# Kernel optimization log

Measured on AMD Instinct MI355X. Metric: run time of the kernel, lower is better.

The kernel has to match this reference:

```python
import jax, jax.numpy as jnp
import numpy as np

N_EMBD = 1024
HEAD_SIZE = 64
B, T = 8, 2048


def setup_inputs() -> dict:
    key = jax.random.key(0)
    kx, kq, kk, kv = jax.random.split(key, 4)
    s = 1.0 / np.sqrt(N_EMBD)  # ~ torch Linear init scale
    return {
        "x": jax.random.normal(kx, (B, T, N_EMBD), dtype=jnp.float32),
        "Wq": jax.random.normal(kq, (N_EMBD, HEAD_SIZE), dtype=jnp.float32) * s,
        "Wk": jax.random.normal(kk, (N_EMBD, HEAD_SIZE), dtype=jnp.float32) * s,
        "Wv": jax.random.normal(kv, (N_EMBD, HEAD_SIZE), dtype=jnp.float32) * s,
    }


def reference(x, Wq, Wk, Wv):
    # x: [B,T,C]; single-head causal self-attention (dropout p=0.0 / eval)
    q = jnp.einsum("btc,cd->btd", x, Wq)
    k = jnp.einsum("btc,cd->btd", x, Wk)
    v = jnp.einsum("btc,cd->btd", x, Wv)
    scale = 1.0 / np.sqrt(HEAD_SIZE).astype(np.float32)
    scores = jnp.einsum("bqd,bkd->bqk", q, k) * scale  # [B,T,T]
    Tq = x.shape[1]
    causal = jnp.tril(jnp.ones((Tq, Tq), dtype=bool))
    scores = jnp.where(causal[None, :, :], scores, -jnp.inf)
    attn = jax.nn.softmax(scores, axis=-1)
    out = jnp.einsum("bqk,bkd->bqd", attn, v)  # [B,T,head_size]
    return out
```

## Files before the change

### kernel.cpp

```cpp
#include <hip/hip_runtime.h>
#include <hip/hip_bf16.h>

#define BATCH 8
#define SEQ   2048
#define CDIM  1024
#define HDIM  64
#define NROWS (BATCH*SEQ)
#define NSPLIT 8

typedef __attribute__((ext_vector_type(8))) short bf16x8;
typedef __attribute__((ext_vector_type(4))) float f32x4;

#define QSCALE 0.18033688011112042f
#define SFIX 24.0f

__device__ inline ushort f2bf(float f) {
    union { float f; uint u; } x; x.f = f;
    uint r = (x.u + 0x7fffu + ((x.u >> 16) & 1u)) >> 16;
    return (ushort)r;
}

__global__ __launch_bounds__(256) void wpack_kernel(
    const float* __restrict__ Wq, const float* __restrict__ Wk,
    const float* __restrict__ Wv, ushort* __restrict__ wp)
{
    __shared__ ushort lt[64][132];
    const int which = blockIdx.x >> 3;
    const int cblk  = blockIdx.x & 7;
    const float* W = (which == 0) ? Wq : (which == 1) ? Wk : Wv;
    const float sc = (which == 0) ? QSCALE : 1.0f;
    const int t = threadIdx.x;
    const float4* Wb = reinterpret_cast<const float4*>(W + (size_t)cblk * 128 * 64);
    #pragma unroll
    for (int j = 0; j < 8; ++j) {
        const int off4 = j * 256 + t;
        float4 v = Wb[off4];
        const int c = off4 >> 4;
        const int n0 = (off4 & 15) * 4;
        lt[n0 + 0][c] = f2bf(v.x * sc);
        lt[n0 + 1][c] = f2bf(v.y * sc);
        lt[n0 + 2][c] = f2bf(v.z * sc);
        lt[n0 + 3][c] = f2bf(v.w * sc);
    }
    __syncthreads();
    const int n = t >> 2, cq = (t & 3) * 32;
    ushort* dst = wp + (size_t)(which * 64 + n) * CDIM + cblk * 128 + cq;
    #pragma unroll
    for (int k = 0; k < 32; ++k) dst[k] = lt[n][cq + k];
}

__global__ __launch_bounds__(512, 4) void qkv_gemm(
    const float* __restrict__ x, const ushort* __restrict__ wp,
    ushort* __restrict__ qb, ushort* __restrict__ kbuf, ushort* __restrict__ vt)
{
    __shared__ ushort xs[2][32 * 64];
    __shared__ ushort ws[2][192 * 64];
    const int t = threadIdx.x;
    const int w = t >> 6, lane = t & 63;
    const int l15 = lane & 15, hi = lane >> 4;
    const int rowg = w & 1, colg = w >> 1;
    const int m0 = blockIdx.x * 32;

    f32x4 acc[3];
    #pragma unroll
    for (int i = 0; i < 3; ++i) acc[i] = (f32x4){0.f, 0.f, 0.f, 0.f};

    const int xrow = t >> 4, xc4 = t & 15;
    const int wn0 = t >> 3,          wc0 = t & 7;
    const int wn1 = (t + 512) >> 3,  wc1 = (t + 512) & 7;
    const int wn2 = (t + 1024) >> 3, wc2 = (t + 1024) & 7;

    float4 xra, xrb;
    uint4 wra0, wra1, wra2, wrb0, wrb1, wrb2;

#define LOADS(S, KK)                                                           \
    xr##S = reinterpret_cast<const float4*>(x + (size_t)(m0 + xrow) * CDIM + (KK))[xc4]; \
    wr##S##0 = reinterpret_cast<const uint4*>(wp + (size_t)wn0 * CDIM + (KK))[wc0]; \
    wr##S##1 = reinterpret_cast<const uint4*>(wp + (size_t)wn1 * CDIM + (KK))[wc1]; \
    wr##S##2 = reinterpret_cast<const uint4*>(wp + (size_t)wn2 * CDIM + (KK))[wc2];

#define WRITES(S, BUF)                                                         \
    {                                                                          \
        ushort4 bx = make_ushort4(f2bf(xr##S.x), f2bf(xr##S.y), f2bf(xr##S.z), f2bf(xr##S.w)); \
        int xb = (xrow * 128 + xc4 * 8) ^ ((xrow & 7) << 4);                   \
        *reinterpret_cast<ushort4*>(reinterpret_cast<char*>(xs[BUF]) + xb) = bx; \
        int y0 = (wn0 * 128 + wc0 * 16) ^ ((wn0 & 7) << 4);                    \
        int y1 = (wn1 * 128 + wc1 * 16) ^ ((wn1 & 7) << 4);                    \
        int y2 = (wn2 * 128 + wc2 * 16) ^ ((wn2 & 7) << 4);                    \
        *reinterpret_cast<uint4*>(reinterpret_cast<char*>(ws[BUF]) + y0) = wr##S##0; \
        *reinterpret_cast<uint4*>(reinterpret_cast<char*>(ws[BUF]) + y1) = wr##S##1; \
        *reinterpret_cast<uint4*>(reinterpret_cast<char*>(ws[BUF]) + y2) = wr##S##2; \
    }

#define MFMA_STEP(BUF)                                                         \
    {                                                                          \
        const int arow = rowg * 16 + l15;                                      \
        _Pragma("unroll")                                                      \
        for (int c32 = 0; c32 < 2; ++c32) {                                    \
            const int abyte = (arow * 128 + hi * 16 + c32 * 64) ^ ((arow & 7) << 4); \
            bf16x8 a = *reinterpret_cast<const bf16x8*>(reinterpret_cast<char*>(xs[BUF]) + abyte); \
            _Pragma("unroll")                                                  \
            for (int nf = 0; nf < 3; ++nf) {                                   \
                const int n = colg * 48 + nf * 16 + l15;                       \
                const int bbyte = (n * 128 + hi * 16 + c32 * 64) ^ ((n & 7) << 4); \
                bf16x8 b = *reinterpret_cast<const bf16x8*>(reinterpret_cast<char*>(ws[BUF]) + bbyte); \
                acc[nf] = __builtin_amdgcn_mfma_f32_16x16x32_bf16(a, b, acc[nf], 0, 0, 0); \
            }                                                                  \
        }                                                                      \
    }

    LOADS(a, 0)
    LOADS(b, 64)
    WRITES(a, 0)
    __syncthreads();

    for (int step = 0; step < 16; step += 2) {
        if (step + 2 < 16) { LOADS(a, (step + 2) * 64) }
        MFMA_STEP(0)
        WRITES(b, 1)
        __syncthreads();
        if (step + 3 < 16) { LOADS(b, (step + 3) * 64) }
        MFMA_STEP(1)
        if (step + 2 < 16) { WRITES(a, 0) }
        __syncthreads();
    }
#undef LOADS
#undef WRITES
#undef MFMA_STEP

    #pragma unroll
    for (int nf = 0; nf < 3; ++nf) {
        const int n = colg * 48 + nf * 16 + l15;
        #pragma unroll
        for (int r = 0; r < 4; ++r) {
            const int grow = m0 + rowg * 16 + hi * 4 + r;
            const ushort bv = f2bf(acc[nf][r]);
            if (n < 64) {
                qb[(size_t)grow * 64 + n] = bv;
            } else if (n < 128) {
                kbuf[(size_t)grow * 64 + (n - 64)] = bv;
            } else {
                const int b = grow >> 11, tt = grow & 2047;
                vt[(((size_t)b * 64 + (n - 128)) << 11) + tt] = bv;
            }
        }
    }
}

__global__ __launch_bounds__(256, 4) void attn_flash(
    const ushort* __restrict__ qb, const ushort* __restrict__ kbuf,
    const ushort* __restrict__ vt, ushort* __restrict__ Opart,
    float* __restrict__ lpart)
{
    __shared__ ushort kst[2][64 * 64];
    __shared__ ushort vst[2][64 * 64];
    __shared__ ushort P[4][1024];

    const int t = threadIdx.x;
    const int w = t >> 6, lane = t & 63;
    const int l15 = lane & 15, hi = lane >> 4;
    const int bid = blockIdx.x;
    const int pid = (bid & 7) * 128 + (bid >> 3);
    const int batch = pid >> 7;
    const int rem = pid & 127;
    const int pairIdx = rem >> 3;
    const int s = rem & 7;
    const int qtA = pairIdx, qtB = 31 - pairIdx;
    const int ntA = qtA + 1;

    const ushort* kB = kbuf + (size_t)batch * SEQ * 64;
    const ushort* vB = vt + (size_t)batch * 64 * SEQ;
    ushort* Osp = Opart + (size_t)s * NROWS * 64;
    float* lsp = lpart + (size_t)s * NROWS;
    char* pw = reinterpret_cast<char*>(P[w]);

    const int r0 = t >> 3, c8 = t & 7;
    const int r1 = r0 + 32;
    const int sb0 = (r0 * 128 + c8 * 16) ^ ((r0 & 7) << 4);
    const int sb1 = (r1 * 128 + c8 * 16) ^ ((r1 & 7) << 4);

    uint4 kr0, kr1, vr0, vr1;

#define STAGE_ISSUE(C)                                                        \
    {                                                                         \
        const int kt_ = ((C) >= ntA) ? ((C) - ntA) : (C);                     \
        const int j0_ = kt_ * 64;                                             \
        kr0 = *reinterpret_cast<const uint4*>(kB + (size_t)(j0_ + r0) * 64 + c8 * 8); \
        kr1 = *reinterpret_cast<const uint4*>(kB + (size_t)(j0_ + r1) * 64 + c8 * 8); \
        vr0 = *reinterpret_cast<const uint4*>(vB + (size_t)r0 * SEQ + j0_ + c8 * 8);  \
        vr1 = *reinterpret_cast<const uint4*>(vB + (size_t)r1 * SEQ + j0_ + c8 * 8);  \
    }

#define STAGE_WRITE(BUF)                                                      \
    {                                                                         \
        *reinterpret_cast<uint4*>(reinterpret_cast<char*>(kst[BUF]) + sb0) = kr0; \
        *reinterpret_cast<uint4*>(reinterpret_cast<char*>(kst[BUF]) + sb1) = kr1; \
        *reinterpret_cast<uint4*>(reinterpret_cast<char*>(vst[BUF]) + sb0) = vr0; \
        *reinterpret_cast<uint4*>(reinterpret_cast<char*>(vst[BUF]) + sb1) = vr1; \
    }

#define LOADQ(QT)                                                             \
    {                                                                         \
        const ushort* qp_ = qb + (size_t)(batch * SEQ + (QT) * 64 + w * 16 + l15) * 64 + hi * 8; \
        aq0 = *reinterpret_cast<const bf16x8*>(qp_);                          \
        aq1 = *reinterpret_cast<const bf16x8*>(qp_ + 32);                     \
    }

#define DUMP(QT)                                                              \
    {                                                                         \
        _Pragma("unroll")                                                     \
        for (int dt = 0; dt < 4; ++dt)                                        \
            _Pragma("unroll")                                                 \
            for (int r = 0; r < 4; ++r)                                       \
                Osp[(size_t)(batch * SEQ + (QT) * 64 + w * 16 + hi * 4 + r) * 64 + dt * 16 + l15] = f2bf(O[dt][r]); \
        _Pragma("unroll")                                                     \
        for (int r = 0; r < 4; ++r) {                                         \
            float s_ = lsum[r];                                               \
            s_ += __shfl_xor(s_, 1, 64);                                      \
            s_ += __shfl_xor(s_, 2, 64);                                      \
            s_ += __shfl_xor(s_, 4, 64);                                      \
            s_ += __shfl_xor(s_, 8, 64);                                      \
            if (l15 == 0)                                                     \
                lsp[batch * SEQ + (QT) * 64 + w * 16 + hi * 4 + r] = s_;      \
        }                                                                     \
    }

#define RESET_STATE()                                                         \
    {                                                                         \
        _Pragma("unroll")                                                     \
        for (int i = 0; i < 4; ++i) {                                         \
            O[i] = (f32x4){0.f, 0.f, 0.f, 0.f};                               \
            lsum[i] = 0.f;                                                    \
        }                                                                     \
    }

    bf16x8 aq0, aq1;
    LOADQ(qtA)
    f32x4 O[4];
    float lsum[4];
    RESET_STATE()

    STAGE_ISSUE(s)
    STAGE_WRITE(0)
    __syncthreads();

    int curB = 0, cur = 0;
    for (int c = s; c < 33; c += 8) {
        if (c + 8 < 33) { STAGE_ISSUE(c + 8) }
        if (c >= ntA && !curB) {
            DUMP(qtA)
            RESET_STATE()
            LOADQ(qtB)
            curB = 1;
        }
        const int qt = curB ? qtB : qtA;
        const int kt = curB ? (c - ntA) : c;
        const int j0 = kt * 64;
        const int qrow0 = qt * 64 + w * 16;
        const bool diag = curB ? (c == 32) : (c == ntA - 1);

        const char* kc = reinterpret_cast<const char*>(kst[cur]);
        const char* vc = reinterpret_cast<const char*>(vst[cur]);

        f32x4 S[4];
        #pragma unroll
        for (int kb = 0; kb < 4; ++kb) {
            const int key = kb * 16 + l15;
            const int sw = (key & 7) << 4;
            bf16x8 b0 = *reinterpret_cast<const bf16x8*>(kc + ((key * 128 + hi * 16) ^ sw));
            bf16x8 b1 = *reinterpret_cast<const bf16x8*>(kc + ((key * 128 + hi * 16 + 64) ^ sw));
            f32x4 z = (f32x4){0.f, 0.f, 0.f, 0.f};
            z = __builtin_amdgcn_mfma_f32_16x16x32_bf16(aq0, b0, z, 0, 0, 0);
            z = __builtin_amdgcn_mfma_f32_16x16x32_bf16(aq1, b1, z, 0, 0, 0);
            S[kb] = z;
        }
        if (diag) {
            #pragma unroll
            for (int kb = 0; kb < 4; ++kb) {
                const int key = j0 + kb * 16 + l15;
                #pragma unroll
                for (int r = 0; r < 4; ++r) {
                    const int qr = qrow0 + hi * 4 + r;
                    if (key > qr) S[kb][r] = -1e30f;
                }
            }
        }
        #pragma unroll
        for (int kb = 0; kb < 4; ++kb)
            #pragma unroll
            for (int r = 0; r < 4; ++r)
                S[kb][r] = exp2f(S[kb][r] - SFIX);
        #pragma unroll
        for (int r = 0; r < 4; ++r)
            lsum[r] += (S[0][r] + S[1][r]) + (S[2][r] + S[3][r]);

        #pragma unroll
        for (int kb = 0; kb < 4; ++kb) {
            #pragma unroll
            for (int r = 0; r < 4; ++r) {
                const int prow = hi * 4 + r;
                const int pcol = kb * 16 + l15;
                const int byte = (prow * 128 + pcol * 2) ^ ((prow & 7) << 4);
                *reinterpret_cast<ushort*>(pw + byte) = f2bf(S[kb][r]);
            }
        }
        asm volatile("" ::: "memory");
        const int pb0 = (l15 * 128 + hi * 16) ^ ((l15 & 7) << 4);
        const int pb1 = (l15 * 128 + hi * 16 + 64) ^ ((l15 & 7) << 4);
        bf16x8 pa0 = *reinterpret_cast<const bf16x8*>(pw + pb0);
        bf16x8 pa1 = *reinterpret_cast<const bf16x8*>(pw + pb1);
        #pragma unroll
        for (int dt = 0; dt < 4; ++dt) {
            const int d = dt * 16 + l15;
            const int sw = (d & 7) << 4;
            bf16x8 v0 = *reinterpret_cast<const bf16x8*>(vc + ((d * 128 + hi * 16) ^ sw));
            bf16x8 v1 = *reinterpret_cast<const bf16x8*>(vc + ((d * 128 + hi * 16 + 64) ^ sw));
            O[dt] = __builtin_amdgcn_mfma_f32_16x16x32_bf16(pa0, v0, O[dt], 0, 0, 0);
            O[dt] = __builtin_amdgcn_mfma_f32_16x16x32_bf16(pa1, v1, O[dt], 0, 0, 0);
        }
        if (c + 8 < 33) { STAGE_WRITE(cur ^ 1) }
        __syncthreads();
        cur ^= 1;
    }

    DUMP(qtB)
#undef STAGE_ISSUE
#undef STAGE_WRITE
#undef LOADQ
#undef DUMP
#undef RESET_STATE
}

__global__ __launch_bounds__(256) void merge_kernel(
    const ushort* __restrict__ Opart, const float* __restrict__ lpart,
    float* __restrict__ out)
{
    const int idx = blockIdx.x * 256 + threadIdx.x;
    const int row = idx >> 3;
    float acc[8] = {0.f, 0.f, 0.f, 0.f, 0.f, 0.f, 0.f, 0.f};
    float lv = 0.f;
    #pragma unroll
    for (int s = 0; s < NSPLIT; ++s) {
        uint4 v = reinterpret_cast<const uint4*>(Opart + (size_t)s * NROWS * 64)[idx];
        const uint u0 = v.x, u1 = v.y, u2 = v.z, u3 = v.w;
        acc[0] += __uint_as_float((u0 & 0xffffu) << 16);
        acc[1] += __uint_as_float(u0 & 0xffff0000u);
        acc[2] += __uint_as_float((u1 & 0xffffu) << 16);
        acc[3] += __uint_as_float(u1 & 0xffff0000u);
        acc[4] += __uint_as_float((u2 & 0xffffu) << 16);
        acc[5] += __uint_as_float(u2 & 0xffff0000u);
        acc[6] += __uint_as_float((u3 & 0xffffu) << 16);
        acc[7] += __uint_as_float(u3 & 0xffff0000u);
        lv += lpart[s * NROWS + row];
    }
    const float inv = 1.0f / lv;
    float4 o0 = make_float4(acc[0] * inv, acc[1] * inv, acc[2] * inv, acc[3] * inv);
    float4 o1 = make_float4(acc[4] * inv, acc[5] * inv, acc[6] * inv, acc[7] * inv);
    reinterpret_cast<float4*>(out)[idx * 2]     = o0;
    reinterpret_cast<float4*>(out)[idx * 2 + 1] = o1;
}

extern "C" void kernel_launch(void* const* d_in, const int* in_sizes, int n_in,
                              void* d_out, int out_size, void* d_ws, size_t ws_size,
                              hipStream_t stream) {
    const float* x  = (const float*)d_in[0];
    const float* Wq = (const float*)d_in[1];
    const float* Wk = (const float*)d_in[2];
    const float* Wv = (const float*)d_in[3];
    float* out = (float*)d_out;

    ushort* qb   = (ushort*)d_ws;
    ushort* kbuf = qb + (size_t)NROWS * 64;
    ushort* vt   = kbuf + (size_t)NROWS * 64;
    ushort* wp   = vt + (size_t)NROWS * 64;
    float* lpart = (float*)(wp + 192 * 1024);
    ushort* Opart = (ushort*)(lpart + (size_t)NSPLIT * NROWS);

    wpack_kernel<<<24, 256, 0, stream>>>(Wq, Wk, Wv, wp);
    qkv_gemm<<<NROWS / 32, 512, 0, stream>>>(x, wp, qb, kbuf, vt);
    attn_flash<<<1024, 256, 0, stream>>>(qb, kbuf, vt, Opart, lpart);
    merge_kernel<<<(NROWS * HDIM / 8) / 256, 256, 0, stream>>>(Opart, lpart, out);
}
```

Before: 51.37 us.

## Pre-swizzle weights into MFMA fragment order and load B operands directly from global

```diff
diff --git a/kernel.cpp b/kernel.cpp
--- a/kernel.cpp
+++ b/kernel.cpp
@@ -22,39 +22,37 @@
 
 __global__ __launch_bounds__(256) void wpack_kernel(
     const float* __restrict__ Wq, const float* __restrict__ Wk,
-    const float* __restrict__ Wv, ushort* __restrict__ wp)
+    const float* __restrict__ Wv, ushort* __restrict__ wp2)
 {
-    __shared__ ushort lt[64][132];
-    const int which = blockIdx.x >> 3;
-    const int cblk  = blockIdx.x & 7;
+    const int g = blockIdx.x * 256 + threadIdx.x;
+    const int l15  = g & 15;
+    const int hi   = (g >> 4) & 3;
+    const int c32  = (g >> 6) & 1;
+    const int step = (g >> 7) & 15;
+    const int f    = g >> 11;
+    const int n = f * 16 + l15;
+    const int which = n >> 6, nl = n & 63;
     const float* W = (which == 0) ? Wq : (which == 1) ? Wk : Wv;
     const float sc = (which == 0) ? QSCALE : 1.0f;
-    const int t = threadIdx.x;
-    const float4* Wb = reinterpret_cast<const float4*>(W + (size_t)cblk * 128 * 64);
+    const int c0 = step * 64 + c32 * 32 + hi * 8;
+
+    ushort v[8];
     #pragma unroll
-    for (int j = 0; j < 8; ++j) {
-        const int off4 = j * 256 + t;
-        float4 v = Wb[off4];
-        const int c = off4 >> 4;
-        const int n0 = (off4 & 15) * 4;
-        lt[n0 + 0][c] = f2bf(v.x * sc);
-        lt[n0 + 1][c] = f2bf(v.y * sc);
-        lt[n0 + 2][c] = f2bf(v.z * sc);
-        lt[n0 + 3][c] = f2bf(v.w * sc);
-    }
-    __syncthreads();
-    const int n = t >> 2, cq = (t & 3) * 32;
-    ushort* dst = wp + (size_t)(which * 64 + n) * CDIM + cblk * 128 + cq;
-    #pragma unroll
-    for (int k = 0; k < 32; ++k) dst[k] = lt[n][cq + k];
+    for (int j = 0; j < 8; ++j)
+        v[j] = f2bf(W[(size_t)(c0 + j) * HDIM + nl] * sc);
+    uint4 pack;
+    pack.x = (uint)v[0] | ((uint)v[1] << 16);
+    pack.y = (uint)v[2] | ((uint)v[3] << 16);
+    pack.z = (uint)v[4] | ((uint)v[5] << 16);
+    pack.w = (uint)v[6] | ((uint)v[7] << 16);
+    reinterpret_cast<uint4*>(wp2)[g] = pack;
 }
 
 __global__ __launch_bounds__(512, 4) void qkv_gemm(
-    const float* __restrict__ x, const ushort* __restrict__ wp,
+    const float* __restrict__ x, const ushort* __restrict__ wp2,
     ushort* __restrict__ qb, ushort* __restrict__ kbuf, ushort* __restrict__ vt)
 {
     __shared__ ushort xs[2][32 * 64];
-    __shared__ ushort ws[2][192 * 64];
     const int t = threadIdx.x;
     const int w = t >> 6, lane = t & 63;
     const int l15 = lane & 15, hi = lane >> 4;
@@ -66,66 +64,56 @@
     for (int i = 0; i < 3; ++i) acc[i] = (f32x4){0.f, 0.f, 0.f, 0.f};
 
     const int xrow = t >> 4, xc4 = t & 15;
-    const int wn0 = t >> 3,          wc0 = t & 7;
-    const int wn1 = (t + 512) >> 3,  wc1 = (t + 512) & 7;
-    const int wn2 = (t + 1024) >> 3, wc2 = (t + 1024) & 7;
-
     float4 xra, xrb;
-    uint4 wra0, wra1, wra2, wrb0, wrb1, wrb2;
-
-#define LOADS(S, KK)                                                           \
-    xr##S = reinterpret_cast<const float4*>(x + (size_t)(m0 + xrow) * CDIM + (KK))[xc4]; \
-    wr##S##0 = reinterpret_cast<const uint4*>(wp + (size_t)wn0 * CDIM + (KK))[wc0]; \
-    wr##S##1 = reinterpret_cast<const uint4*>(wp + (size_t)wn1 * CDIM + (KK))[wc1]; \
-    wr##S##2 = reinterpret_cast<const uint4*>(wp + (size_t)wn2 * CDIM + (KK))[wc2];
-
-#define WRITES(S, BUF)                                                         \
+    const ushort* wbase = wp2 + (size_t)lane * 8;
+
+#define LOADX(S, KK)                                                           \
+    xr##S = reinterpret_cast<const float4*>(x + (size_t)(m0 + xrow) * CDIM + (KK))[xc4];
+
+#define WRITEX(S, BUF)                                                         \
     {                                                                          \
         ushort4 bx = make_ushort4(f2bf(xr##S.x), f2bf(xr##S.y), f2bf(xr##S.z), f2bf(xr##S.w)); \
         int xb = (xrow * 128 + xc4 * 8) ^ ((xrow & 7) << 4);                   \
         *reinterpret_cast<ushort4*>(reinterpret_cast<char*>(xs[BUF]) + xb) = bx; \
-        int y0 = (wn0 * 128 + wc0 * 16) ^ ((wn0 & 7) << 4);                    \
-        int y1 = (wn1 * 128 + wc1 * 16) ^ ((wn1 & 7) << 4);                    \
-        int y2 = (wn2 * 128 + wc2 * 16) ^ ((wn2 & 7) << 4);                    \
-        *reinterpret_cast<uint4*>(reinterpret_cast<char*>(ws[BUF]) + y0) = wr##S##0; \
-        *reinterpret_cast<uint4*>(reinterpret_cast<char*>(ws[BUF]) + y1) = wr##S##1; \
-        *reinterpret_cast<uint4*>(reinterpret_cast<char*>(ws[BUF]) + y2) = wr##S##2; \
-    }
-
-#define MFMA_STEP(BUF)                                                         \
+    }
+
+#define MFMA_STEP(BUF, STEP)                                                   \
     {                                                                          \
         const int arow = rowg * 16 + l15;                                      \
+        bf16x8 bf[6];                                                          \
+        _Pragma("unroll")                                                      \
+        for (int nf = 0; nf < 3; ++nf) {                                       \
+            const int f = colg * 3 + nf;                                       \
+            bf[nf * 2 + 0] = *reinterpret_cast<const bf16x8*>(wbase + (size_t)(f * 16 + (STEP)) * 1024);       \
+            bf[nf * 2 + 1] = *reinterpret_cast<const bf16x8*>(wbase + (size_t)(f * 16 + (STEP)) * 1024 + 512); \
+        }                                                                      \
         _Pragma("unroll")                                                      \
         for (int c32 = 0; c32 < 2; ++c32) {                                    \
             const int abyte = (arow * 128 + hi * 16 + c32 * 64) ^ ((arow & 7) << 4); \
             bf16x8 a = *reinterpret_cast<const bf16x8*>(reinterpret_cast<char*>(xs[BUF]) + abyte); \
             _Pragma("unroll")                                                  \
-            for (int nf = 0; nf < 3; ++nf) {                                   \
-                const int n = colg * 48 + nf * 16 + l15;                       \
-                const int bbyte = (n * 128 + hi * 16 + c32 * 64) ^ ((n & 7) << 4); \
-                bf16x8 b = *reinterpret_cast<const bf16x8*>(reinterpret_cast<char*>(ws[BUF]) + bbyte); \
-                acc[nf] = __builtin_amdgcn_mfma_f32_16x16x32_bf16(a, b, acc[nf], 0, 0, 0); \
-            }                                                                  \
+            for (int nf = 0; nf < 3; ++nf)                                     \
+                acc[nf] = __builtin_amdgcn_mfma_f32_16x16x32_bf16(a, bf[nf * 2 + c32], acc[nf], 0, 0, 0); \
         }                                                                      \
     }
 
-    LOADS(a, 0)
-    LOADS(b, 64)
-    WRITES(a, 0)
+    LOADX(a, 0)
+    LOADX(b, 64)
+    WRITEX(a, 0)
     __syncthreads();
 
     for (int step = 0; step < 16; step += 2) {
-        if (step + 2 < 16) { LOADS(a, (step + 2) * 64) }
-        MFMA_STEP(0)
-        WRITES(b, 1)
+        if (step + 2 < 16) { LOADX(a, (step + 2) * 64) }
+        MFMA_STEP(0, step)
+        WRITEX(b, 1)
         __syncthreads();
-        if (step + 3 < 16) { LOADS(b, (step + 3) * 64) }
-        MFMA_STEP(1)
-        if (step + 2 < 16) { WRITES(a, 0) }
+        if (step + 3 < 16) { LOADX(b, (step + 3) * 64) }
+        MFMA_STEP(1, step + 1)
+        if (step + 2 < 16) { WRITEX(a, 0) }
         __syncthreads();
     }
-#undef LOADS
-#undef WRITES
+#undef LOADX
+#undef WRITEX
 #undef MFMA_STEP
 
     #pragma unroll
@@ -372,12 +360,12 @@
     ushort* qb   = (ushort*)d_ws;
     ushort* kbuf = qb + (size_t)NROWS * 64;
     ushort* vt   = kbuf + (size_t)NROWS * 64;
-    ushort* wp   = vt + (size_t)NROWS * 64;
-    float* lpart = (float*)(wp + 192 * 1024);
+    ushort* wp2  = vt + (size_t)NROWS * 64;
+    float* lpart = (float*)(wp2 + 192 * 1024);
     ushort* Opart = (ushort*)(lpart + (size_t)NSPLIT * NROWS);
 
-    wpack_kernel<<<24, 256, 0, stream>>>(Wq, Wk, Wv, wp);
-    qkv_gemm<<<NROWS / 32, 512, 0, stream>>>(x, wp, qb, kbuf, vt);
+    wpack_kernel<<<96, 256, 0, stream>>>(Wq, Wk, Wv, wp2);
+    qkv_gemm<<<NROWS / 32, 512, 0, stream>>>(x, wp2, qb, kbuf, vt);
     attn_flash<<<1024, 256, 0, stream>>>(qb, kbuf, vt, Opart, lpart);
     merge_kernel<<<(NROWS * HDIM / 8) / 256, 256, 0, stream>>>(Opart, lpart, out);
 }
```

New measurement: 53.40 us. 1.04x slower.

## Fuse split-K merge into attention kernel via last-block atomic counter

Applied to the files above, without the earlier changes.

```diff
diff --git a/kernel.cpp b/kernel.cpp
--- a/kernel.cpp
+++ b/kernel.cpp
@@ -51,11 +51,15 @@
 
 __global__ __launch_bounds__(512, 4) void qkv_gemm(
     const float* __restrict__ x, const ushort* __restrict__ wp,
-    ushort* __restrict__ qb, ushort* __restrict__ kbuf, ushort* __restrict__ vt)
+    ushort* __restrict__ qb, ushort* __restrict__ kbuf, ushort* __restrict__ vt,
+    uint* __restrict__ cnt)
 {
     __shared__ ushort xs[2][32 * 64];
     __shared__ ushort ws[2][192 * 64];
     const int t = threadIdx.x;
+
+    if (blockIdx.x == 0 && t < 128) cnt[t] = 0u;
+
     const int w = t >> 6, lane = t & 63;
     const int l15 = lane & 15, hi = lane >> 4;
     const int rowg = w & 1, colg = w >> 1;
@@ -150,11 +154,13 @@
 __global__ __launch_bounds__(256, 4) void attn_flash(
     const ushort* __restrict__ qb, const ushort* __restrict__ kbuf,
     const ushort* __restrict__ vt, ushort* __restrict__ Opart,
-    float* __restrict__ lpart)
+    float* __restrict__ lpart, float* __restrict__ out,
+    uint* __restrict__ cnt)
 {
     __shared__ ushort kst[2][64 * 64];
     __shared__ ushort vst[2][64 * 64];
     __shared__ ushort P[4][1024];
+    __shared__ int lastFlag;
 
     const int t = threadIdx.x;
     const int w = t >> 6, lane = t & 63;
@@ -329,35 +335,47 @@
 #undef LOADQ
 #undef DUMP
 #undef RESET_STATE
-}
-
-__global__ __launch_bounds__(256) void merge_kernel(
-    const ushort* __restrict__ Opart, const float* __restrict__ lpart,
-    float* __restrict__ out)
-{
-    const int idx = blockIdx.x * 256 + threadIdx.x;
-    const int row = idx >> 3;
-    float acc[8] = {0.f, 0.f, 0.f, 0.f, 0.f, 0.f, 0.f, 0.f};
-    float lv = 0.f;
-    #pragma unroll
-    for (int s = 0; s < NSPLIT; ++s) {
-        uint4 v = reinterpret_cast<const uint4*>(Opart + (size_t)s * NROWS * 64)[idx];
-        const uint u0 = v.x, u1 = v.y, u2 = v.z, u3 = v.w;
-        acc[0] += __uint_as_float((u0 & 0xffffu) << 16);
-        acc[1] += __uint_as_float(u0 & 0xffff0000u);
-        acc[2] += __uint_as_float((u1 & 0xffffu) << 16);
-        acc[3] += __uint_as_float(u1 & 0xffff0000u);
-        acc[4] += __uint_as_float((u2 & 0xffffu) << 16);
-        acc[5] += __uint_as_float(u2 & 0xffff0000u);
-        acc[6] += __uint_as_float((u3 & 0xffffu) << 16);
-        acc[7] += __uint_as_float(u3 & 0xffff0000u);
-        lv += lpart[s * NROWS + row];
-    }
-    const float inv = 1.0f / lv;
-    float4 o0 = make_float4(acc[0] * inv, acc[1] * inv, acc[2] * inv, acc[3] * inv);
-    float4 o1 = make_float4(acc[4] * inv, acc[5] * inv, acc[6] * inv, acc[7] * inv);
-    reinterpret_cast<float4*>(out)[idx * 2]     = o0;
-    reinterpret_cast<float4*>(out)[idx * 2 + 1] = o1;
+
+    __threadfence();
+    __syncthreads();
+    if (t == 0) {
+        const uint old = atomicAdd(&cnt[batch * 16 + pairIdx], 1u);
+        lastFlag = (old == 7u) ? 1 : 0;
+    }
+    __syncthreads();
+    if (lastFlag) {
+        __threadfence();
+        for (int task = t; task < 1024; task += 256) {
+            const int tile = task >> 9;
+            const int row  = (task >> 3) & 63;
+            const int cg   = task & 7;
+            const int qt   = tile ? qtB : qtA;
+            const int grow = batch * SEQ + qt * 64 + row;
+            float acc[8] = {0.f, 0.f, 0.f, 0.f, 0.f, 0.f, 0.f, 0.f};
+            float lv = 0.f;
+            #pragma unroll
+            for (int s2 = 0; s2 < NSPLIT; ++s2) {
+                const uint4 v = *reinterpret_cast<const uint4*>(
+                    Opart + ((size_t)s2 * NROWS + grow) * 64 + cg * 8);
+                const uint u0 = v.x, u1 = v.y, u2 = v.z, u3 = v.w;
+                acc[0] += __uint_as_float((u0 & 0xffffu) << 16);
+                acc[1] += __uint_as_float(u0 & 0xffff0000u);
+                acc[2] += __uint_as_float((u1 & 0xffffu) << 16);
+                acc[3] += __uint_as_float(u1 & 0xffff0000u);
+                acc[4] += __uint_as_float((u2 & 0xffffu) << 16);
+                acc[5] += __uint_as_float(u2 & 0xffff0000u);
+                acc[6] += __uint_as_float((u3 & 0xffffu) << 16);
+                acc[7] += __uint_as_float(u3 & 0xffff0000u);
+                lv += lpart[s2 * NROWS + grow];
+            }
+            const float inv = 1.0f / lv;
+            float4 o0 = make_float4(acc[0] * inv, acc[1] * inv, acc[2] * inv, acc[3] * inv);
+            float4 o1 = make_float4(acc[4] * inv, acc[5] * inv, acc[6] * inv, acc[7] * inv);
+            float* op = out + (size_t)grow * 64 + cg * 8;
+            *reinterpret_cast<float4*>(op)     = o0;
+            *reinterpret_cast<float4*>(op + 4) = o1;
+        }
+    }
 }
 
 extern "C" void kernel_launch(void* const* d_in, const int* in_sizes, int n_in,
@@ -375,9 +393,9 @@
     ushort* wp   = vt + (size_t)NROWS * 64;
     float* lpart = (float*)(wp + 192 * 1024);
     ushort* Opart = (ushort*)(lpart + (size_t)NSPLIT * NROWS);
+    uint* cnt = (uint*)(Opart + (size_t)NSPLIT * NROWS * 64);
 
     wpack_kernel<<<24, 256, 0, stream>>>(Wq, Wk, Wv, wp);
-    qkv_gemm<<<NROWS / 32, 512, 0, stream>>>(x, wp, qb, kbuf, vt);
-    attn_flash<<<1024, 256, 0, stream>>>(qb, kbuf, vt, Opart, lpart);
-    merge_kernel<<<(NROWS * HDIM / 8) / 256, 256, 0, stream>>>(Opart, lpart, out);
+    qkv_gemm<<<NROWS / 32, 512, 0, stream>>>(x, wp, qb, kbuf, vt, cnt);
+    attn_flash<<<1024, 256, 0, stream>>>(qb, kbuf, vt, Opart, lpart, out, cnt);
 }
```

After: 177.5 us. 246% more time.
